# Kernel tuning notes

Hardware: AMD Instinct MI355X
Metric: run time of the kernel (lower is better)

The kernel has to match this reference:

```python
import jax, jax.numpy as jnp
import numpy as np

TEMP = 20.0
NEG = -1.0e9


def l2norm(x, eps=1e-12):
    # F.normalize(p=2, dim=-1): x / max(||x||, eps)
    n = jnp.sqrt(jnp.sum(x * x, axis=-1, keepdims=True))
    return x / jnp.maximum(n, eps)


def setup_inputs() -> dict:
    key = jax.random.key(0)
    ks = jax.random.split(key, 8)
    Bv, Lv, Dv = 32, 196, 768
    Bt, Lt, Dt = 32, 64, 768
    D = 512
    inp = {
        "visual_feature": jax.random.normal(ks[0], (Bv, Lv, Dv), jnp.float32),
        "textual_feature": jax.random.normal(ks[1], (Bt, Lt, Dt), jnp.float32),
        "mask": jax.random.randint(ks[2], (Bt, Lt), 0, 2, jnp.int32),
        "W_vis": jax.random.normal(ks[3], (D, Dv), jnp.float32) * (2.0 / D) ** 0.5,
        "b_vis": jnp.zeros((D,), jnp.float32),
        "W_txt": jax.random.normal(ks[4], (D, Dt), jnp.float32) * (2.0 / D) ** 0.5,
        "b_txt": jnp.zeros((D,), jnp.float32),
        "W_qs": jax.random.normal(ks[5], (D, D), jnp.float32) * (2.0 / D) ** 0.5,
        "W_ks": jax.random.normal(ks[6], (D, D), jnp.float32) * (2.0 / D) ** 0.5,
    }
    return inp


def _mha(q_in, k_in, v_in, k_mask, W_qs, W_ks):
    # all-pairs cross attention (n_head == 1), vectorized over the original
    # per-sample Python loop: output [Bk, Bq, Lq, Dv]
    q = l2norm(jnp.einsum('qld,ed->qle', q_in, W_qs))  # [Bq, Lq, D]
    k = l2norm(jnp.einsum('kmd,ed->kme', k_in, W_ks))  # [Bk, Lk, D]
    attn = jnp.einsum('qle,kme->kqlm', q, k)           # [Bk, Bq, Lq, Lk]
    attn = jax.nn.relu(attn) * TEMP
    if k_mask is not None:
        attn = jnp.where(k_mask[:, None, None, :] == 1, NEG, attn)
    attn = jax.nn.softmax(attn, axis=-1)
    return jnp.einsum('kqlm,kmd->kqld', attn, v_in)    # [Bk, Bq, Lq, Dv]


def reference(visual_feature, textual_feature, mask, W_vis, b_vis, W_txt, b_txt, W_qs, W_ks):
    visual_embed = jnp.einsum('bld,ed->ble', visual_feature, W_vis) + b_vis   # [Bv,Lv,D]
    textual_embed = jnp.einsum('bld,ed->ble', textual_feature, W_txt) + b_txt # [Bt,Lt,D]
    visual_norm = l2norm(visual_embed)
    textual_norm = l2norm(textual_embed)
    # q=visual, k/v=textual, masked by text padding -> [Bt, Bv, Lv, D]
    att_text = _mha(visual_norm, textual_norm, textual_embed, mask, W_qs, W_ks)
    # q=textual, k/v=visual, no mask -> [Bv, Bt, Lt, D]
    att_vis = _mha(textual_norm, visual_norm, visual_embed, None, W_qs, W_ks)
    att_text = l2norm(att_text)
    att_vis = l2norm(att_vis)
    # att_vis_feat[:, mask == 1, :] = 0
    att_vis = att_vis * (mask == 0)[None, :, :, None].astype(att_vis.dtype)
    # matmul(att_text [t,v,l,d], att_vis.permute(1,0,3,2) [t,v,d,m]) -> mean(2,3)
    sim = jnp.einsum('tvld,vtmd->tvlm', att_text, att_vis)
    return sim.mean(axis=(2, 3))  # [Bt, Bv]
```

## Files before the change

### kernel.cpp

```cpp
#include <hip/hip_runtime.h>
#include <math.h>

#define BV 32
#define LV 196
#define DV 768
#define BT 32
#define LT 64
#define DD 512
#define MV (BV*LV)
#define MT (BT*LT)
#define TEMPF 20.0f
#define NEGF  -1.0e9f

typedef unsigned short u16;
typedef unsigned int   u32;
typedef short bf16x8 __attribute__((ext_vector_type(8)));
typedef float f32x4  __attribute__((ext_vector_type(4)));

__device__ __forceinline__ u16 f2bf(float f) {
    u32 u = __float_as_uint(f);
    u32 r = u + 0x7fffu + ((u >> 16) & 1u);
    return (u16)(r >> 16);
}
__device__ __forceinline__ float bf2f(u16 h) { return __uint_as_float(((u32)h) << 16); }

__device__ __forceinline__ size_t tiled_chunk_off(int m, int kk, int KB2) {
    int rowBlk = m >> 7, row = m & 127;
    int kBlk = kk >> 6, ke = kk & 63;
    return ((size_t)(rowBlk * KB2 + kBlk) << 13) + row * 64 + ((((ke >> 3) ^ (row & 7)) << 4) >> 1);
}

__global__ __launch_bounds__(256)
void conv_split(const float* __restrict__ X, u16* __restrict__ X2, int M, int K)
{
    int gid = blockIdx.x * 256 + threadIdx.x;
    int perRow = K >> 3;
    if (gid >= M * perRow) return;
    int m = gid / perRow, k8 = (gid - m * perRow) << 3;
    const float* xp = X + (size_t)m * K + k8;
    float x[8];
    *(float4*)&x[0] = *(const float4*)xp;
    *(float4*)&x[4] = *(const float4*)(xp + 4);
    union { u16 h[8]; uint4 v; } hi, lo;
    #pragma unroll
    for (int e = 0; e < 8; ++e) {
        hi.h[e] = f2bf(x[e]);
        lo.h[e] = f2bf(x[e] - bf2f(hi.h[e]));
    }
    int KB2 = K >> 5;
    *(uint4*)&X2[tiled_chunk_off(m, k8, KB2)]     = hi.v;
    *(uint4*)&X2[tiled_chunk_off(m, K + k8, KB2)] = lo.v;
}

__global__ __launch_bounds__(256)
void rownorm_conv(const float* __restrict__ X, u16* __restrict__ X2, int M)
{
    const int row  = blockIdx.x * 4 + (threadIdx.x >> 6);
    const int lane = threadIdx.x & 63;
    const float* ip = X + (size_t)row * DD + lane * 8;
    float x[8];
    *(float4*)&x[0] = *(const float4*)ip;
    *(float4*)&x[4] = *(const float4*)(ip + 4);
    float ss = 0.f;
    #pragma unroll
    for (int e = 0; e < 8; ++e) ss += x[e] * x[e];
    #pragma unroll
    for (int off = 32; off; off >>= 1) ss += __shfl_xor(ss, off, 64);
    const float inv = 1.f / fmaxf(sqrtf(ss), 1e-12f);
    union { u16 h[8]; uint4 v; } hi, lo;
    #pragma unroll
    for (int e = 0; e < 8; ++e) {
        float xv = x[e] * inv;
        hi.h[e] = f2bf(xv);
        lo.h[e] = f2bf(xv - bf2f(hi.h[e]));
    }
    const int k8 = lane * 8, KB2 = 16;
    *(uint4*)&X2[tiled_chunk_off(row, k8, KB2)]       = hi.v;
    *(uint4*)&X2[tiled_chunk_off(row, DD + k8, KB2)]  = lo.v;
}

__device__ __forceinline__ void gload16(const u16* g, u16* l) {
    __builtin_amdgcn_global_load_lds((const __attribute__((address_space(1))) u32*)g,
                                     (__attribute__((address_space(3))) u32*)l, 16, 0, 0);
}

__global__ __launch_bounds__(256, 2)
void gemm_split_nt(const u16* __restrict__ A2, const u16* __restrict__ B2,
                   const float* __restrict__ bias, float* __restrict__ C,
                   int M, int N, int K, int hasBias, int split)
{
    const int KB  = K >> 6;
    const int KB2 = KB * 2;
    const int bm = blockIdx.y, bn = blockIdx.x;
    const int tid = threadIdx.x;
    const int w = tid >> 6, lane = tid & 63;
    const int wr = (w >> 1) << 6, wc = (w & 1) << 6;
    const int fr = lane & 15, fq = lane >> 4;

    __shared__ u16 As[2][8192];
    __shared__ u16 Bs[2][8192];

    f32x4 acc[4][4];
    #pragma unroll
    for (int i = 0; i < 4; ++i)
        #pragma unroll
        for (int j = 0; j < 4; ++j) acc[i][j] = (f32x4){0.f, 0.f, 0.f, 0.f};

    const int swz = (fr & 7) << 4;
    const int aoff0 = ((wr + fr) << 7) >> 1;
    const int boff0 = ((wc + fr) << 7) >> 1;
    const int k0 = ((fq << 4) ^ swz) >> 1;
    const int k1 = ((64 + (fq << 4)) ^ swz) >> 1;

    const int c4 = w * 4;
    const int laneOff = c4 * 512 + lane * 8;

    const int T = split ? 3 * KB : KB;
    int cur = 0;

    {
        const u16* ag = A2 + (((size_t)(bm * KB2)) << 13) + laneOff;
        const u16* bg = B2 + (((size_t)(bn * KB2)) << 13) + laneOff;
        #pragma unroll
        for (int i = 0; i < 4; ++i) {
            gload16(ag + i * 512, &As[0][(c4 + i) * 512]);
            gload16(bg + i * 512, &Bs[0][(c4 + i) * 512]);
        }
    }
    __syncthreads();

    for (int t = 0; t < T; ++t) {
        if (t + 1 < T) {
            int tn = t + 1, ab, bb;
            if (tn < KB)           { ab = tn;          bb = tn; }
            else if (tn < 2 * KB)  { ab = tn - KB;     bb = tn; }
            else                   { ab = tn - KB;     bb = tn - 2 * KB; }
            const u16* ag = A2 + (((size_t)(bm * KB2 + ab)) << 13) + laneOff;
            const u16* bg = B2 + (((size_t)(bn * KB2 + bb)) << 13) + laneOff;
            int nb = cur ^ 1;
            #pragma unroll
            for (int i = 0; i < 4; ++i) {
                gload16(ag + i * 512, &As[nb][(c4 + i) * 512]);
                gload16(bg + i * 512, &Bs[nb][(c4 + i) * 512]);
            }
        }
        #pragma unroll
        for (int ks = 0; ks < 2; ++ks) {
            const int kk = ks ? k1 : k0;
            bf16x8 af[4], bfv[4];
            #pragma unroll
            for (int mi = 0; mi < 4; ++mi)
                af[mi] = *(const bf16x8*)&As[cur][aoff0 + mi * 1024 + kk];
            #pragma unroll
            for (int ni = 0; ni < 4; ++ni)
                bfv[ni] = *(const bf16x8*)&Bs[cur][boff0 + ni * 1024 + kk];
            #pragma unroll
            for (int mi = 0; mi < 4; ++mi)
                #pragma unroll
                for (int ni = 0; ni < 4; ++ni)
                    acc[mi][ni] = __builtin_amdgcn_mfma_f32_16x16x32_bf16(
                        af[mi], bfv[ni], acc[mi][ni], 0, 0, 0);
        }
        __syncthreads();
        cur ^= 1;
    }

    #pragma unroll
    for (int ni = 0; ni < 4; ++ni) {
        const int col = (bn << 7) + wc + ni * 16 + fr;
        const float badd = hasBias ? bias[col] : 0.f;
        #pragma unroll
        for (int mi = 0; mi < 4; ++mi) {
            #pragma unroll
            for (int j = 0; j < 4; ++j) {
                const int row = (bm << 7) + wr + mi * 16 + fq * 4 + j;
                C[(size_t)row * N + col] = acc[mi][ni][j] + badd;
            }
        }
    }
}

__global__ __launch_bounds__(256, 2)
void gemm_pg(const u16* __restrict__ P, const u16* __restrict__ G,
             float* __restrict__ U)
{
    const int v = blockIdx.z;
    const int bm = blockIdx.y, bn = blockIdx.x;
    const int tid = threadIdx.x;
    const int w = tid >> 6, lane = tid & 63;
    const int wr = (w >> 1) << 6, wc = (w & 1) << 6;
    const int fr = lane & 15, fq = lane >> 4;

    const u16* A2 = P + ((size_t)v << 19);
    const u16* B2 = G + ((size_t)v << 16);

    __shared__ u16 As[2][8192];
    __shared__ u16 Bs[2][8192];

    f32x4 acc[4][4];
    #pragma unroll
    for (int i = 0; i < 4; ++i)
        #pragma unroll
        for (int j = 0; j < 4; ++j) acc[i][j] = (f32x4){0.f, 0.f, 0.f, 0.f};

    const int swz = (fr & 7) << 4;
    const int aoff0 = ((wr + fr) << 7) >> 1;
    const int boff0 = ((wc + fr) << 7) >> 1;
    const int k0 = ((fq << 4) ^ swz) >> 1;
    const int k1 = ((64 + (fq << 4)) ^ swz) >> 1;
    const int c4 = w * 4;
    const int laneOff = c4 * 512 + lane * 8;

    int cur = 0;
    {
        const u16* ag = A2 + (((size_t)(bm * 4)) << 13) + laneOff;
        const u16* bg = B2 + (((size_t)(bn * 4)) << 13) + laneOff;
        #pragma unroll
        for (int i = 0; i < 4; ++i) {
            gload16(ag + i * 512, &As[0][(c4 + i) * 512]);
            gload16(bg + i * 512, &Bs[0][(c4 + i) * 512]);
        }
    }
    __syncthreads();

    for (int t = 0; t < 4; ++t) {
        if (t + 1 < 4) {
            const u16* ag = A2 + (((size_t)(bm * 4 + t + 1)) << 13) + laneOff;
            const u16* bg = B2 + (((size_t)(bn * 4 + t + 1)) << 13) + laneOff;
            int nb = cur ^ 1;
            #pragma unroll
            for (int i = 0; i < 4; ++i) {
                gload16(ag + i * 512, &As[nb][(c4 + i) * 512]);
                gload16(bg + i * 512, &Bs[nb][(c4 + i) * 512]);
            }
        }
        #pragma unroll
        for (int ks = 0; ks < 2; ++ks) {
            const int kk = ks ? k1 : k0;
            bf16x8 af[4], bfv[4];
            #pragma unroll
            for (int mi = 0; mi < 4; ++mi)
                af[mi] = *(const bf16x8*)&As[cur][aoff0 + mi * 1024 + kk];
            #pragma unroll
            for (int ni = 0; ni < 4; ++ni)
                bfv[ni] = *(const bf16x8*)&Bs[cur][boff0 + ni * 1024 + kk];
            #pragma unroll
            for (int mi = 0; mi < 4; ++mi)
                #pragma unroll
                for (int ni = 0; ni < 4; ++ni)
                    acc[mi][ni] = __builtin_amdgcn_mfma_f32_16x16x32_bf16(
                        af[mi], bfv[ni], acc[mi][ni], 0, 0, 0);
        }
        __syncthreads();
        cur ^= 1;
    }

    float* Uv = U + (size_t)v * MT * 196;
    #pragma unroll
    for (int ni = 0; ni < 4; ++ni) {
        const int col = (bn << 7) + wc + ni * 16 + fr;
        if (col < 196) {
            #pragma unroll
            for (int mi = 0; mi < 4; ++mi) {
                #pragma unroll
                for (int j = 0; j < 4; ++j) {
                    const int row = (bm << 7) + wr + mi * 16 + fq * 4 + j;
                    Uv[(size_t)row * 196 + col] = acc[mi][ni][j];
                }
            }
        }
    }
}

__global__ __launch_bounds__(256)
void gram_text(const float* __restrict__ X, u16* __restrict__ Gtp,
               float* __restrict__ diagT)
{
    const int bat = blockIdx.z;
    const int tid = threadIdx.x;
    const int tx = tid & 15, ty = tid >> 4;
    __shared__ float Xa[32][68];
    const float* Xbase = X + (size_t)bat * 64 * DD;

    float acc[4][4];
    #pragma unroll
    for (int i = 0; i < 4; ++i)
        #pragma unroll
        for (int j = 0; j < 4; ++j) acc[i][j] = 0.f;

    for (int k0 = 0; k0 < DD; k0 += 32) {
        {
            int idx = tid;
            #pragma unroll
            for (int i = 0; i < 2; ++i) {
                int id2 = idx + 256 * i;
                int row = id2 >> 3;
                int kc  = (id2 & 7) << 2;
                float4 av = *(const float4*)(Xbase + (size_t)row * DD + k0 + kc);
                Xa[kc + 0][row] = av.x; Xa[kc + 1][row] = av.y;
                Xa[kc + 2][row] = av.z; Xa[kc + 3][row] = av.w;
            }
        }
        __syncthreads();
        #pragma unroll 8
        for (int kk = 0; kk < 32; ++kk) {
            float a[4], b[4];
            *(float4*)a = *(const float4*)&Xa[kk][ty * 4];
            *(float4*)b = *(const float4*)&Xa[kk][tx * 4];
            #pragma unroll
            for (int i = 0; i < 4; ++i)
                #pragma unroll
                for (int j = 0; j < 4; ++j)
                    acc[i][j] = fmaf(a[i], b[j], acc[i][j]);
        }
        __syncthreads();
    }

    u16* Gv = Gtp + ((size_t)bat << 12);
    #pragma unroll
    for (int i = 0; i < 4; ++i) {
        const int row = ty * 4 + i;
        #pragma unroll
        for (int jj = 0; jj < 4; ++jj) {
            const int col = tx * 4 + jj;
            float val = acc[i][jj];
            Gv[row * 64 + ((((col >> 3) ^ (row & 7)) << 3) | (col & 7))] =
                (row != col) ? f2bf(val) : (u16)0;
            if (row == col) diagT[bat * 64 + row] = val;
        }
    }
}

__global__ __launch_bounds__(256)
void gram_vis(const float* __restrict__ X, u16* __restrict__ Gp,
              float* __restrict__ diagF)
{
    const int bat = blockIdx.z;
    const int it = blockIdx.y, jt = blockIdx.x;
    const int tid = threadIdx.x;
    const int tx = tid & 15, ty = tid >> 4;
    __shared__ float Xa[32][68];
    __shared__ float Xb[32][68];
    const float* Xbase = X + (size_t)bat * 196 * DD;

    float acc[4][4];
    #pragma unroll
    for (int i = 0; i < 4; ++i)
        #pragma unroll
        for (int j = 0; j < 4; ++j) acc[i][j] = 0.f;

    for (int k0 = 0; k0 < DD; k0 += 32) {
        #pragma unroll
        for (int i = 0; i < 2; ++i) {
            int idx = tid + 256 * i;
            int row = idx >> 3;
            int kc  = (idx & 7) << 2;
            int ra = it * 64 + row; ra = (ra < 196) ? ra : 195;
            int rb = jt * 64 + row; rb = (rb < 196) ? rb : 195;
            float4 av = *(const float4*)(Xbase + (size_t)ra * DD + k0 + kc);
            Xa[kc + 0][row] = av.x; Xa[kc + 1][row] = av.y;
            Xa[kc + 2][row] = av.z; Xa[kc + 3][row] = av.w;
            float4 bv = *(const float4*)(Xbase + (size_t)rb * DD + k0 + kc);
            Xb[kc + 0][row] = bv.x; Xb[kc + 1][row] = bv.y;
            Xb[kc + 2][row] = bv.z; Xb[kc + 3][row] = bv.w;
        }
        __syncthreads();
        #pragma unroll 8
        for (int kk = 0; kk < 32; ++kk) {
            float a[4], b[4];
            *(float4*)a = *(const float4*)&Xa[kk][ty * 4];
            *(float4*)b = *(const float4*)&Xb[kk][tx * 4];
            #pragma unroll
            for (int i = 0; i < 4; ++i)
                #pragma unroll
                for (int j = 0; j < 4; ++j)
                    acc[i][j] = fmaf(a[i], b[j], acc[i][j]);
        }
        __syncthreads();
    }

    u16* Gv = Gp + ((size_t)bat << 16);
    #pragma unroll
    for (int i = 0; i < 4; ++i) {
        const int row = it * 64 + ty * 4 + i;
        #pragma unroll
        for (int jj = 0; jj < 4; ++jj) {
            const int col = jt * 64 + tx * 4 + jj;
            float val = acc[i][jj];
            u16 o = (row < 196 && col < 196 && row != col) ? f2bf(val) : (u16)0;
            Gv[tiled_chunk_off(row, col & ~7, 4) + (col & 7)] = o;
            if (row == col && row < 196) diagF[bat * 196 + row] = val;
        }
    }
}

__global__ __launch_bounds__(256)
void zero_wt(float* __restrict__ WT)
{
    WT[blockIdx.x * 256 + threadIdx.x] = 0.f;
}

__global__ __launch_bounds__(256, 2)
void text_fused(const float* __restrict__ S1, const u16* __restrict__ Gtp,
                const float* __restrict__ diagT, const int* __restrict__ mask,
                float* __restrict__ WT)
{
    const int rb = blockIdx.x;
    const int t  = blockIdx.y;
    const int tid = threadIdx.x;
    const int w = tid >> 6, lane = tid & 63;
    const int fr = lane & 15, fq = lane >> 4;

    __shared__ float Sblk[128 * 64];
    __shared__ u16   Ap[128 * 64];
    __shared__ u16   Glds[64 * 64];
    __shared__ float dsh[64];
    __shared__ float wacc[4][2][64];

    gload16(Gtp + ((size_t)t << 12) + tid * 8,        &Glds[tid * 8]);
    gload16(Gtp + ((size_t)t << 12) + 2048 + tid * 8, &Glds[2048 + tid * 8]);
    if (tid < 64) dsh[tid] = diagT[t * 64 + tid];
    {
        const float* sbase = S1 + (size_t)(rb * 128) * MT + t * 64;
        #pragma unroll
        for (int i = 0; i < 8; ++i) {
            int idx = tid + i * 256;
            int row = idx >> 4, c4 = (idx & 15) << 2;
            *(float4*)&Sblk[row * 64 + c4] = *(const float4*)(sbase + (size_t)row * MT + c4);
        }
    }
    wacc[w][0][lane] = 0.f; wacc[w][1][lane] = 0.f;
    const int mk = mask[t * 64 + lane];
    __syncthreads();

    for (int rr = w; rr < 128; rr += 4) {
        float s = Sblk[rr * 64 + lane];
        float logit = mk ? NEGF : fmaxf(s, 0.f) * TEMPF;
        float mx = logit;
        #pragma unroll
        for (int off = 32; off; off >>= 1) mx = fmaxf(mx, __shfl_xor(mx, off, 64));
        float p = __expf(logit - mx);
        float sum = p;
        #pragma unroll
        for (int off = 32; off; off >>= 1) sum += __shfl_xor(sum, off, 64);
        p /= sum;
        Ap[rr * 64 + ((((lane >> 3) ^ (rr & 7)) << 3) | (lane & 7))] = f2bf(p);
    }
    __syncthreads();

    const int wr = (w >> 1) << 6, wc = (w & 1) << 5;
    f32x4 acc[4][2];
    #pragma unroll
    for (int i = 0; i < 4; ++i) { acc[i][0] = (f32x4){0,0,0,0}; acc[i][1] = (f32x4){0,0,0,0}; }
    const int swz = (fr & 7) << 4;
    const int aoff0 = (wr + fr) * 64;
    const int boff0 = (wc + fr) * 64;
    const int k0 = ((fq << 4) ^ swz) >> 1;
    const int k1 = ((64 + (fq << 4)) ^ swz) >> 1;
    #pragma unroll
    for (int ks = 0; ks < 2; ++ks) {
        const int kk = ks ? k1 : k0;
        bf16x8 af[4], bfv[2];
        #pragma unroll
        for (int mi = 0; mi < 4; ++mi)
            af[mi] = *(const bf16x8*)&Ap[aoff0 + mi * 1024 + kk];
        #pragma unroll
        for (int ni = 0; ni < 2; ++ni)
            bfv[ni] = *(const bf16x8*)&Glds[boff0 + ni * 1024 + kk];
        #pragma unroll
        for (int mi = 0; mi < 4; ++mi)
            #pragma unroll
            for (int ni = 0; ni < 2; ++ni)
                acc[mi][ni] = __builtin_amdgcn_mfma_f32_16x16x32_bf16(
                    af[mi], bfv[ni], acc[mi][ni], 0, 0, 0);
    }
    float* Ulds = Sblk;
    #pragma unroll
    for (int ni = 0; ni < 2; ++ni)
        #pragma unroll
        for (int mi = 0; mi < 4; ++mi)
            #pragma unroll
            for (int j = 0; j < 4; ++j)
                Ulds[(wr + mi * 16 + fq * 4 + j) * 64 + (wc + ni * 16 + fr)] = acc[mi][ni][j];
    __syncthreads();

    const int vb = ((rb * 128) / 196 + 1) * 196;
    for (int rr = w; rr < 128; rr += 4) {
        int r = rb * 128 + rr;
        float p = bf2f(Ap[rr * 64 + ((((lane >> 3) ^ (rr & 7)) << 3) | (lane & 7))]);
        float u = Ulds[rr * 64 + lane];
        float nsq = p * (u + dsh[lane] * p);
        #pragma unroll
        for (int off = 32; off; off >>= 1) nsq += __shfl_xor(nsq, off, 64);
        float inv = 1.f / fmaxf(sqrtf(fmaxf(nsq, 0.f)), 1e-12f);
        int slot = (r >= vb) ? 1 : 0;
        wacc[w][slot][lane] += p * inv;
    }
    __syncthreads();
    if (tid < 128) {
        int slot = tid >> 6, m = tid & 63;
        int v = (rb * 128) / 196 + slot;
        if (v < 32) {
            float val = wacc[0][slot][m] + wacc[1][slot][m] + wacc[2][slot][m] + wacc[3][slot][m];
            atomicAdd(&WT[((size_t)t * 32 + v) * 64 + m], val);
        }
    }
}

__global__ __launch_bounds__(256)
void text_a(const float* __restrict__ WT, const float* __restrict__ TE,
            float* __restrict__ aacc)
{
    const int t = blockIdx.x, v = blockIdx.y;
    const int tid = threadIdx.x;
    __shared__ float wl[64];
    if (tid < 64) wl[tid] = WT[((size_t)t * 32 + v) * 64 + tid];
    __syncthreads();
    const int d = tid * 2;
    float a0 = 0.f, a1 = 0.f;
    const float* tb = TE + (size_t)(t * 64) * DD + d;
    for (int m = 0; m < 64; ++m) {
        float wm = wl[m];
        float2 te = *(const float2*)(tb + (size_t)m * DD);
        a0 = fmaf(wm, te.x, a0);
        a1 = fmaf(wm, te.y, a1);
    }
    *(float2*)(aacc + ((size_t)t * 32 + v) * DD + d) = make_float2(a0, a1);
}

__global__ __launch_bounds__(256)
void softmax_vis(const float* __restrict__ S2, u16* __restrict__ P)
{
    const int row  = blockIdx.x;
    const int wave = threadIdx.x >> 6, lane = threadIdx.x & 63;
    const int v = blockIdx.y * 4 + wave;
    __shared__ float pl[4][256];

    const float* srow = S2 + (size_t)row * MV + v * 196;
    float l0 = fmaxf(srow[lane], 0.f) * TEMPF;
    float l1 = fmaxf(srow[lane + 64], 0.f) * TEMPF;
    float l2 = fmaxf(srow[lane + 128], 0.f) * TEMPF;
    float l3 = -3.0e38f;
    if (lane < 4) l3 = fmaxf(srow[lane + 192], 0.f) * TEMPF;
    float mx = fmaxf(fmaxf(l0, l1), fmaxf(l2, l3));
    #pragma unroll
    for (int off = 32; off; off >>= 1) mx = fmaxf(mx, __shfl_xor(mx, off, 64));
    float p0 = __expf(l0 - mx), p1 = __expf(l1 - mx), p2 = __expf(l2 - mx);
    float p3 = (lane < 4) ? __expf(l3 - mx) : 0.f;
    float sum = p0 + p1 + p2 + p3;
    #pragma unroll
    for (int off = 32; off; off >>= 1) sum += __shfl_xor(sum, off, 64);
    float rs = 1.f / sum;
    pl[wave][lane]       = p0 * rs;
    pl[wave][lane + 64]  = p1 * rs;
    pl[wave][lane + 128] = p2 * rs;
    if (lane < 4) pl[wave][lane + 192] = p3 * rs;
    else          pl[wave][lane + 192] = 0.f;
    __syncthreads();

    if (lane < 32) {
        union { u16 h[8]; uint4 u; } c;
        #pragma unroll
        for (int e = 0; e < 8; ++e) c.h[e] = f2bf(pl[wave][lane * 8 + e]);
        u16* Pv = P + ((size_t)v << 19);
        *(uint4*)&Pv[tiled_chunk_off(row, lane * 8, 4)] = c.u;
    }
}

__global__ __launch_bounds__(256)
void vis_norm_w(const float* __restrict__ U, const u16* __restrict__ P,
                const float* __restrict__ diagF, const int* __restrict__ mask,
                float* __restrict__ Wbuf)
{
    const int t = blockIdx.x, v = blockIdx.y;
    const int wave = threadIdx.x >> 6, lane = threadIdx.x & 63;
    __shared__ float wacc[4][200];

    for (int j = lane; j < 200; j += 64) wacc[wave][j] = 0.f;
    __syncthreads();

    const u16* Pv = P + ((size_t)v << 19);
    const float* dF = diagF + v * 196;
    const float d0 = dF[lane], d1 = dF[lane + 64], d2 = dF[lane + 128];
    const float d3 = (lane < 4) ? dF[lane + 192] : 0.f;

    for (int m = wave; m < 64; m += 4) {
        const int row = t * 64 + m;
        const float* urow = U + ((size_t)v * MT + row) * 196;
        float p0 = bf2f(Pv[tiled_chunk_off(row, lane & ~7, 4) + (lane & 7)]);
        float p1 = bf2f(Pv[tiled_chunk_off(row, (lane + 64) & ~7, 4) + (lane & 7)]);
        float p2 = bf2f(Pv[tiled_chunk_off(row, (lane + 128) & ~7, 4) + (lane & 7)]);
        float p3 = (lane < 4) ? bf2f(Pv[tiled_chunk_off(row, (lane + 192) & ~7, 4) + (lane & 7)]) : 0.f;
        float u0 = urow[lane], u1 = urow[lane + 64], u2 = urow[lane + 128];
        float u3 = (lane < 4) ? urow[lane + 192] : 0.f;
        float nsq = p0 * (u0 + d0 * p0) + p1 * (u1 + d1 * p1)
                  + p2 * (u2 + d2 * p2) + p3 * (u3 + d3 * p3);
        #pragma unroll
        for (int off = 32; off; off >>= 1) nsq += __shfl_xor(nsq, off, 64);
        float inv = 1.f / fmaxf(sqrtf(fmaxf(nsq, 0.f)), 1e-12f);
        if (mask[row]) inv = 0.f;
        wacc[wave][lane]       += p0 * inv;
        wacc[wave][lane + 64]  += p1 * inv;
        wacc[wave][lane + 128] += p2 * inv;
        if (lane < 4) wacc[wave][lane + 192] += p3 * inv;
    }
    __syncthreads();
    const int tid = threadIdx.x;
    if (tid < 196)
        Wbuf[((size_t)v * 32 + t) * 196 + tid] =
            wacc[0][tid] + wacc[1][tid] + wacc[2][tid] + wacc[3][tid];
}

__global__ __launch_bounds__(512)
void vis_b(const float* __restrict__ Wbuf, const float* __restrict__ VE,
           float* __restrict__ bacc)
{
    const int t = blockIdx.x, v = blockIdx.y;
    const int tid = threadIdx.x;
    __shared__ float wl[196];
    if (tid < 196) wl[tid] = Wbuf[((size_t)v * 32 + t) * 196 + tid];
    __syncthreads();
    float a0 = 0.f, a1 = 0.f;
    const float* vb = VE + (size_t)v * 196 * DD + tid;
    for (int j = 0; j < 196; j += 2) {
        a0 = fmaf(wl[j],     vb[(size_t)j * DD],       a0);
        a1 = fmaf(wl[j + 1], vb[(size_t)(j + 1) * DD], a1);
    }
    bacc[((size_t)v * 32 + t) * DD + tid] = a0 + a1;
}

__global__ __launch_bounds__(64)
void final_dot(const float* __restrict__ aacc, const float* __restrict__ bacc,
               float* __restrict__ out)
{
    const int t = blockIdx.x, v = blockIdx.y;
    const int lane = threadIdx.x;
    const float* ap = aacc + ((size_t)t * 32 + v) * DD + lane * 8;
    const float* bp = bacc + ((size_t)v * 32 + t) * DD + lane * 8;
    float4 a0 = *(const float4*)ap,       a1 = *(const float4*)(ap + 4);
    float4 b0 = *(const float4*)bp,       b1 = *(const float4*)(bp + 4);
    float acc = a0.x*b0.x + a0.y*b0.y + a0.z*b0.z + a0.w*b0.w
              + a1.x*b1.x + a1.y*b1.y + a1.z*b1.z + a1.w*b1.w;
    #pragma unroll
    for (int off = 32; off; off >>= 1) acc += __shfl_xor(acc, off, 64);
    if (lane == 0) out[(size_t)t * 32 + v] = acc * (1.f / 12544.f);
}

extern "C" void kernel_launch(void* const* d_in, const int* in_sizes, int n_in,
                              void* d_out, int out_size, void* d_ws, size_t ws_size,
                              hipStream_t stream)
{
    const float* VF   = (const float*)d_in[0];
    const float* TF   = (const float*)d_in[1];
    const int*   mask = (const int*)  d_in[2];
    const float* Wv   = (const float*)d_in[3];
    const float* bv   = (const float*)d_in[4];
    const float* Wt   = (const float*)d_in[5];
    const float* bt   = (const float*)d_in[6];
    const float* Wq   = (const float*)d_in[7];
    const float* Wk   = (const float*)d_in[8];
    float* out = (float*)d_out;

    float* ws = (float*)d_ws;
    size_t off = 0;
    float* R1 = ws + off; off += (size_t)MV * MT;
    float* R2 = ws + off; off += (size_t)MV * DD + (size_t)MT * DD;
    float* R3 = ws + off; off += (size_t)MV * DD;
    float* R4 = ws + off; off += (size_t)MT * DD;
    float* R5 = ws + off; off += (size_t)MV * DD;
    float* R6 = ws + off; off += (size_t)MT * DD;
    float* VE  = ws + off; off += (size_t)MV * DD;
    float* TE  = ws + off; off += (size_t)MT * DD;
    float* GtR = ws + off; off += (size_t)32 * 64 * 64;
    float* GvR = ws + off; off += (size_t)32 * 196 * 196;
    float* Aac = ws + off; off += (size_t)32 * 32 * DD;
    float* Bac = ws + off; off += (size_t)32 * 32 * DD;

    u16* VF2 = (u16*)R1;
    u16* TF2 = (u16*)R2;
    u16* VN2 = (u16*)R3;  u16* Qv2 = (u16*)R3;
    u16* TN2 = (u16*)R4;  u16* Qt2 = (u16*)R4;
    u16* Wv2 = (u16*)R5;
    u16* Wt2 = Wv2 + (size_t)512 * 1536;
    u16* Wq2 = Wt2 + (size_t)512 * 1536;
    u16* Wk2 = Wq2 + (size_t)512 * 1024;
    u16* Kv2 = (u16*)R5;
    u16* Kt2 = (u16*)R6;
    float* Qv = R1;
    float* Qt = R1 + (size_t)MV * DD;
    float* Kv = R2;
    float* Kt = R2 + (size_t)MV * DD;
    float* S  = R1;
    float* U  = R1;
    u16*   P  = (u16*)R3;
    u16*   Gtp  = (u16*)GtR;
    float* diagT = GtR + 65536;
    u16*   Gp = (u16*)GvR;
    float* diagF = GvR + (size_t)32 * 256 * 256 / 2;
    float* WT    = diagF + 6272;
    float* Wbuf = R2;

    conv_split<<<(MV * 96 + 255) / 256, 256, 0, stream>>>(VF, VF2, MV, 768);
    conv_split<<<(MT * 96 + 255) / 256, 256, 0, stream>>>(TF, TF2, MT, 768);
    conv_split<<<(512 * 96 + 255) / 256, 256, 0, stream>>>(Wv, Wv2, 512, 768);
    conv_split<<<(512 * 96 + 255) / 256, 256, 0, stream>>>(Wt, Wt2, 512, 768);
    conv_split<<<(512 * 64 + 255) / 256, 256, 0, stream>>>(Wq, Wq2, 512, 512);
    conv_split<<<(512 * 64 + 255) / 256, 256, 0, stream>>>(Wk, Wk2, 512, 512);

    gemm_split_nt<<<dim3(4, 49), 256, 0, stream>>>(VF2, Wv2, bv, VE, MV, 512, 768, 1, 1);
    gemm_split_nt<<<dim3(4, 16), 256, 0, stream>>>(TF2, Wt2, bt, TE, MT, 512, 768, 1, 1);

    rownorm_conv<<<MV / 4, 256, 0, stream>>>(VE, VN2, MV);
    rownorm_conv<<<MT / 4, 256, 0, stream>>>(TE, TN2, MT);
    gram_text<<<dim3(1, 1, 32), 256, 0, stream>>>(TE, Gtp, diagT);
    gram_vis<<<dim3(4, 4, 32), 256, 0, stream>>>(VE, Gp, diagF);

    gemm_split_nt<<<dim3(4, 49), 256, 0, stream>>>(VN2, Wq2, nullptr, Qv, MV, 512, 512, 0, 1);
    gemm_split_nt<<<dim3(4, 49), 256, 0, stream>>>(VN2, Wk2, nullptr, Kv, MV, 512, 512, 0, 1);
    gemm_split_nt<<<dim3(4, 16), 256, 0, stream>>>(TN2, Wq2, nullptr, Qt, MT, 512, 512, 0, 1);
    gemm_split_nt<<<dim3(4, 16), 256, 0, stream>>>(TN2, Wk2, nullptr, Kt, MT, 512, 512, 0, 1);

    rownorm_conv<<<MV / 4, 256, 0, stream>>>(Qv, Qv2, MV);
    rownorm_conv<<<MV / 4, 256, 0, stream>>>(Kv, Kv2, MV);
    rownorm_conv<<<MT / 4, 256, 0, stream>>>(Qt, Qt2, MT);
    rownorm_conv<<<MT / 4, 256, 0, stream>>>(Kt, Kt2, MT);

    gemm_split_nt<<<dim3(16, 49), 256, 0, stream>>>(Qv2, Kt2, nullptr, S, MV, MT, 512, 0, 0);
    zero_wt<<<256, 256, 0, stream>>>(WT);
    text_fused<<<dim3(49, 32), 256, 0, stream>>>(S, Gtp, diagT, mask, WT);
    text_a<<<dim3(32, 32), 256, 0, stream>>>(WT, TE, Aac);

    gemm_split_nt<<<dim3(49, 16), 256, 0, stream>>>(Qt2, Kv2, nullptr, S, MT, MV, 512, 0, 0);
    softmax_vis<<<dim3(MT, 8), 256, 0, stream>>>(S, P);
    gemm_pg<<<dim3(2, 16, 32), 256, 0, stream>>>(P, Gp, U);
    vis_norm_w<<<dim3(32, 32), 256, 0, stream>>>(U, P, diagF, mask, Wbuf);
    vis_b<<<dim3(32, 32), 512, 0, stream>>>(Wbuf, VE, Bac);

    final_dot<<<dim3(32, 32), 64, 0, stream>>>(Aac, Bac, out);
}
```

Baseline: 660.5 us.

## Drop softmax normalization before scale-invariant l2norm and retile text_fused to 64 rows

The row max-subtraction and sum-division of both attention softmaxes are removed, because each row's result is later L2-normalized and that normalization cancels any per-row scale. Only the unnormalized exponentials are stored as bf16. text_fused now handles 64-row tiles, with a grid twice as large and a higher occupancy hint. It reads S straight from global memory instead of staging it in LDS, which cuts shared memory use. The risks are exp(20*s) growing large without max subtraction, though cosine scores bound this, and a row where every key is masked giving zeros instead of uniform weights.

```diff
diff --git a/kernel.cpp b/kernel.cpp
--- a/kernel.cpp
+++ b/kernel.cpp
@@ -400,7 +400,7 @@
     WT[blockIdx.x * 256 + threadIdx.x] = 0.f;
 }
 
-__global__ __launch_bounds__(256, 2)
+__global__ __launch_bounds__(256, 4)
 void text_fused(const float* __restrict__ S1, const u16* __restrict__ Gtp,
                 const float* __restrict__ diagT, const int* __restrict__ mask,
                 float* __restrict__ WT)
@@ -411,95 +411,67 @@
     const int w = tid >> 6, lane = tid & 63;
     const int fr = lane & 15, fq = lane >> 4;
 
-    __shared__ float Sblk[128 * 64];
-    __shared__ u16   Ap[128 * 64];
+    __shared__ u16   Ap[64 * 64];
     __shared__ u16   Glds[64 * 64];
+    __shared__ float Ulds[64 * 64];
     __shared__ float dsh[64];
     __shared__ float wacc[4][2][64];
 
     gload16(Gtp + ((size_t)t << 12) + tid * 8,        &Glds[tid * 8]);
     gload16(Gtp + ((size_t)t << 12) + 2048 + tid * 8, &Glds[2048 + tid * 8]);
     if (tid < 64) dsh[tid] = diagT[t * 64 + tid];
-    {
-        const float* sbase = S1 + (size_t)(rb * 128) * MT + t * 64;
-        #pragma unroll
-        for (int i = 0; i < 8; ++i) {
-            int idx = tid + i * 256;
-            int row = idx >> 4, c4 = (idx & 15) << 2;
-            *(float4*)&Sblk[row * 64 + c4] = *(const float4*)(sbase + (size_t)row * MT + c4);
-        }
-    }
     wacc[w][0][lane] = 0.f; wacc[w][1][lane] = 0.f;
     const int mk = mask[t * 64 + lane];
-    __syncthreads();
-
-    for (int rr = w; rr < 128; rr += 4) {
-        float s = Sblk[rr * 64 + lane];
-        float logit = mk ? NEGF : fmaxf(s, 0.f) * TEMPF;
-        float mx = logit;
-        #pragma unroll
-        for (int off = 32; off; off >>= 1) mx = fmaxf(mx, __shfl_xor(mx, off, 64));
-        float p = __expf(logit - mx);
-        float sum = p;
-        #pragma unroll
-        for (int off = 32; off; off >>= 1) sum += __shfl_xor(sum, off, 64);
-        p /= sum;
-        Ap[rr * 64 + ((((lane >> 3) ^ (rr & 7)) << 3) | (lane & 7))] = f2bf(p);
-    }
-    __syncthreads();
-
-    const int wr = (w >> 1) << 6, wc = (w & 1) << 5;
-    f32x4 acc[4][2];
-    #pragma unroll
-    for (int i = 0; i < 4; ++i) { acc[i][0] = (f32x4){0,0,0,0}; acc[i][1] = (f32x4){0,0,0,0}; }
+    const int r0 = rb * 64;
+
+    for (int rr = w; rr < 64; rr += 4) {
+        float s = S1[(size_t)(r0 + rr) * MT + t * 64 + lane];
+        float e = mk ? 0.f : __expf(fmaxf(s, 0.f) * TEMPF);
+        Ap[rr * 64 + ((((lane >> 3) ^ (rr & 7)) << 3) | (lane & 7))] = f2bf(e);
+    }
+    __syncthreads();
+
+    const int wr = w << 4;
+    f32x4 acc[4];
+    #pragma unroll
+    for (int i = 0; i < 4; ++i) acc[i] = (f32x4){0.f, 0.f, 0.f, 0.f};
     const int swz = (fr & 7) << 4;
     const int aoff0 = (wr + fr) * 64;
-    const int boff0 = (wc + fr) * 64;
     const int k0 = ((fq << 4) ^ swz) >> 1;
     const int k1 = ((64 + (fq << 4)) ^ swz) >> 1;
     #pragma unroll
     for (int ks = 0; ks < 2; ++ks) {
         const int kk = ks ? k1 : k0;
-        bf16x8 af[4], bfv[2];
-        #pragma unroll
-        for (int mi = 0; mi < 4; ++mi)
-            af[mi] = *(const bf16x8*)&Ap[aoff0 + mi * 1024 + kk];
-        #pragma unroll
-        for (int ni = 0; ni < 2; ++ni)
-            bfv[ni] = *(const bf16x8*)&Glds[boff0 + ni * 1024 + kk];
-        #pragma unroll
-        for (int mi = 0; mi < 4; ++mi)
-            #pragma unroll
-            for (int ni = 0; ni < 2; ++ni)
-                acc[mi][ni] = __builtin_amdgcn_mfma_f32_16x16x32_bf16(
-                    af[mi], bfv[ni], acc[mi][ni], 0, 0, 0);
-    }
-    float* Ulds = Sblk;
-    #pragma unroll
-    for (int ni = 0; ni < 2; ++ni)
-        #pragma unroll
-        for (int mi = 0; mi < 4; ++mi)
-            #pragma unroll
-            for (int j = 0; j < 4; ++j)
-                Ulds[(wr + mi * 16 + fq * 4 + j) * 64 + (wc + ni * 16 + fr)] = acc[mi][ni][j];
-    __syncthreads();
-
-    const int vb = ((rb * 128) / 196 + 1) * 196;
-    for (int rr = w; rr < 128; rr += 4) {
-        int r = rb * 128 + rr;
-        float p = bf2f(Ap[rr * 64 + ((((lane >> 3) ^ (rr & 7)) << 3) | (lane & 7))]);
+        bf16x8 af = *(const bf16x8*)&Ap[aoff0 + kk];
+        #pragma unroll
+        for (int ni = 0; ni < 4; ++ni) {
+            bf16x8 bfv = *(const bf16x8*)&Glds[(ni * 16 + fr) * 64 + kk];
+            acc[ni] = __builtin_amdgcn_mfma_f32_16x16x32_bf16(af, bfv, acc[ni], 0, 0, 0);
+        }
+    }
+    #pragma unroll
+    for (int ni = 0; ni < 4; ++ni)
+        #pragma unroll
+        for (int j = 0; j < 4; ++j)
+            Ulds[(wr + fq * 4 + j) * 64 + ni * 16 + fr] = acc[ni][j];
+    __syncthreads();
+
+    const int vb = (r0 / 196 + 1) * 196;
+    for (int rr = w; rr < 64; rr += 4) {
+        int r = r0 + rr;
+        float e = bf2f(Ap[rr * 64 + ((((lane >> 3) ^ (rr & 7)) << 3) | (lane & 7))]);
         float u = Ulds[rr * 64 + lane];
-        float nsq = p * (u + dsh[lane] * p);
+        float nsq = e * (u + dsh[lane] * e);
         #pragma unroll
         for (int off = 32; off; off >>= 1) nsq += __shfl_xor(nsq, off, 64);
         float inv = 1.f / fmaxf(sqrtf(fmaxf(nsq, 0.f)), 1e-12f);
         int slot = (r >= vb) ? 1 : 0;
-        wacc[w][slot][lane] += p * inv;
+        wacc[w][slot][lane] += e * inv;
     }
     __syncthreads();
     if (tid < 128) {
         int slot = tid >> 6, m = tid & 63;
-        int v = (rb * 128) / 196 + slot;
+        int v = r0 / 196 + slot;
         if (v < 32) {
             float val = wacc[0][slot][m] + wacc[1][slot][m] + wacc[2][slot][m] + wacc[3][slot][m];
             atomicAdd(&WT[((size_t)t * 32 + v) * 64 + m], val);
@@ -529,7 +501,7 @@
 }
 
 __global__ __launch_bounds__(256)
-void softmax_vis(const float* __restrict__ S2, u16* __restrict__ P)
+void exp_vis(const float* __restrict__ S2, u16* __restrict__ P)
 {
     const int row  = blockIdx.x;
     const int wave = threadIdx.x >> 6, lane = threadIdx.x & 63;
@@ -537,25 +509,10 @@
     __shared__ float pl[4][256];
 
     const float* srow = S2 + (size_t)row * MV + v * 196;
-    float l0 = fmaxf(srow[lane], 0.f) * TEMPF;
-    float l1 = fmaxf(srow[lane + 64], 0.f) * TEMPF;
-    float l2 = fmaxf(srow[lane + 128], 0.f) * TEMPF;
-    float l3 = -3.0e38f;
-    if (lane < 4) l3 = fmaxf(srow[lane + 192], 0.f) * TEMPF;
-    float mx = fmaxf(fmaxf(l0, l1), fmaxf(l2, l3));
-    #pragma unroll
-    for (int off = 32; off; off >>= 1) mx = fmaxf(mx, __shfl_xor(mx, off, 64));
-    float p0 = __expf(l0 - mx), p1 = __expf(l1 - mx), p2 = __expf(l2 - mx);
-    float p3 = (lane < 4) ? __expf(l3 - mx) : 0.f;
-    float sum = p0 + p1 + p2 + p3;
-    #pragma unroll
-    for (int off = 32; off; off >>= 1) sum += __shfl_xor(sum, off, 64);
-    float rs = 1.f / sum;
-    pl[wave][lane]       = p0 * rs;
-    pl[wave][lane + 64]  = p1 * rs;
-    pl[wave][lane + 128] = p2 * rs;
-    if (lane < 4) pl[wave][lane + 192] = p3 * rs;
-    else          pl[wave][lane + 192] = 0.f;
+    pl[wave][lane]       = __expf(fmaxf(srow[lane], 0.f) * TEMPF);
+    pl[wave][lane + 64]  = __expf(fmaxf(srow[lane + 64], 0.f) * TEMPF);
+    pl[wave][lane + 128] = __expf(fmaxf(srow[lane + 128], 0.f) * TEMPF);
+    pl[wave][lane + 192] = (lane < 4) ? __expf(fmaxf(srow[lane + 192], 0.f) * TEMPF) : 0.f;
     __syncthreads();
 
     if (lane < 32) {
@@ -727,11 +684,11 @@
 
     gemm_split_nt<<<dim3(16, 49), 256, 0, stream>>>(Qv2, Kt2, nullptr, S, MV, MT, 512, 0, 0);
     zero_wt<<<256, 256, 0, stream>>>(WT);
-    text_fused<<<dim3(49, 32), 256, 0, stream>>>(S, Gtp, diagT, mask, WT);
+    text_fused<<<dim3(98, 32), 256, 0, stream>>>(S, Gtp, diagT, mask, WT);
     text_a<<<dim3(32, 32), 256, 0, stream>>>(WT, TE, Aac);
 
     gemm_split_nt<<<dim3(49, 16), 256, 0, stream>>>(Qt2, Kv2, nullptr, S, MT, MV, 512, 0, 0);
-    softmax_vis<<<dim3(MT, 8), 256, 0, stream>>>(S, P);
+    exp_vis<<<dim3(MT, 8), 256, 0, stream>>>(S, P);
     gemm_pg<<<dim3(2, 16, 32), 256, 0, stream>>>(P, Gp, U);
     vis_norm_w<<<dim3(32, 32), 256, 0, stream>>>(U, P, diagF, mask, Wbuf);
     vis_b<<<dim3(32, 32), 512, 0, stream>>>(Wbuf, VE, Bac);
```

After: 595.5 us. 1.11x faster.
